# Kernel tuning notes

Hardware: AMD Instinct MI355X
Metric: run time of the kernel (lower is better)

Reference implementation:

```python
import jax, jax.numpy as jnp
import numpy as np

N_ING, N_DIR = 100000, 50000
E = 1000000
H, D = 4, 16          # heads, per-head dim
HID = H * D           # 64
LAT, COND = 32, 8
F_ING, F_DIR = 16, 8
OUT_ING = 16


def _han_edge(x_src, x_dst, att_s, att_d, edge_index, n_dst):
    # HANConv per-edge-type attention message passing.
    src, dst = edge_index[0], edge_index[1]
    a = jax.nn.leaky_relu(
        jnp.einsum('nhd,hd->nh', x_src, att_s)[src]
        + jnp.einsum('nhd,hd->nh', x_dst, att_d)[dst],
        negative_slope=0.2)                               # [E, H]
    amax = jax.ops.segment_max(a, dst, num_segments=n_dst)
    ex = jnp.exp(a - amax[dst])
    denom = jax.ops.segment_sum(ex, dst, num_segments=n_dst)
    alpha = ex / (denom[dst] + 1e-16)                     # PyG softmax eps
    out = jax.ops.segment_sum(x_src[src] * alpha[:, :, None], dst,
                              num_segments=n_dst)         # [n_dst, H, D]
    return jax.nn.relu(out.reshape(n_dst, HID))


def _group(outs, q, Wk, bk):
    # HANConv semantic-level attention across edge types.
    s = jnp.stack(outs)                                   # [T, N, HID]
    score = jnp.tanh(s @ Wk + bk).mean(axis=1) @ q        # [T]
    attn = jax.nn.softmax(score)
    return jnp.einsum('t,tnf->nf', attn, s)


def setup_inputs() -> dict:
    key = jax.random.key(0)
    ks = jax.random.split(key, 32)
    def ei(k, n_src, n_dst):
        k1, k2 = jax.random.split(k)
        return jnp.stack([jax.random.randint(k1, (E,), 0, n_src),
                          jax.random.randint(k2, (E,), 0, n_dst)]).astype(jnp.int64)
    s = 0.1
    inp = {
        'x_ing': jax.random.normal(ks[0], (N_ING, F_ING), jnp.float32),
        'x_dir': jax.random.normal(ks[1], (N_DIR, F_DIR), jnp.float32),
        'cond':  jax.random.normal(ks[2], (COND,), jnp.float32),
        'eps':   jax.random.normal(ks[3], (1, LAT), jnp.float32),
        'ei_cooc':     ei(ks[4], N_ING, N_DIR),
        'ei_used':     ei(ks[5], N_ING, N_DIR),
        'ei_contains': ei(ks[6], N_DIR, N_ING),
        'ei_pairs':    ei(ks[7], N_DIR, N_DIR),
        'ei_follows':  ei(ks[8], N_DIR, N_DIR),
        # node-type projections
        'W_pi': jax.random.normal(ks[9],  (F_ING, HID)) * s,
        'b_pi': jnp.zeros((HID,)),
        'W_pd': jax.random.normal(ks[10], (F_DIR, HID)) * s,
        'b_pd': jnp.zeros((HID,)),
        # semantic attention
        'Wk': jax.random.normal(ks[21], (HID, HID)) * s,
        'bk': jnp.zeros((HID,)),
        'q':  jax.random.normal(ks[22], (HID,)) * s,
        # VAE heads (input: 2*HID + COND)
        'W_mu': jax.random.normal(ks[23], (2 * HID + COND, LAT)) * s,
        'b_mu': jnp.zeros((LAT,)),
        'W_lv': jax.random.normal(ks[24], (2 * HID + COND, LAT)) * s,
        'b_lv': jnp.zeros((LAT,)),
        # decoder (fc1 is dead code in the original forward)
        'W_fc3': jax.random.normal(ks[25], (LAT, HID)) * s,
        'b_fc3': jnp.zeros((HID,)),
        'W_fc2': jax.random.normal(ks[26], (HID, OUT_ING)) * s,
        'b_fc2': jnp.zeros((OUT_ING,)),
    }
    for i, name in enumerate(['cooc', 'used', 'contains', 'pairs', 'follows']):
        inp[f'as_{name}'] = jax.random.normal(ks[11 + i], (H, D)) * s
        inp[f'ad_{name}'] = jax.random.normal(ks[16 + i], (H, D)) * s
    return inp


def reference(x_ing, x_dir, cond, eps,
              ei_cooc, ei_used, ei_contains, ei_pairs, ei_follows,
              W_pi, b_pi, W_pd, b_pd,
              as_cooc, ad_cooc, as_used, ad_used, as_contains, ad_contains,
              as_pairs, ad_pairs, as_follows, ad_follows,
              Wk, bk, q, W_mu, b_mu, W_lv, b_lv,
              W_fc3, b_fc3, W_fc2, b_fc2):
    # node-type projections -> [N, H, D]
    h_ing = (x_ing @ W_pi + b_pi).reshape(N_ING, H, D)
    h_dir = (x_dir @ W_pd + b_pd).reshape(N_DIR, H, D)

    o_cooc = _han_edge(h_ing, h_dir, as_cooc, ad_cooc, ei_cooc, N_DIR)
    o_used = _han_edge(h_ing, h_dir, as_used, ad_used, ei_used, N_DIR)
    o_cont = _han_edge(h_dir, h_ing, as_contains, ad_contains, ei_contains, N_ING)
    o_pair = _han_edge(h_dir, h_dir, as_pairs, ad_pairs, ei_pairs, N_DIR)
    o_foll = _han_edge(h_dir, h_dir, as_follows, ad_follows, ei_follows, N_DIR)

    out_ing = _group([o_cont], q, Wk, bk)                       # [N_ING, HID]
    out_dir = _group([o_cooc, o_used, o_pair, o_foll], q, Wk, bk)

    ingre_pool = out_ing.mean(axis=0, keepdims=True)            # [1, HID]
    direc_pool = out_dir.mean(axis=0, keepdims=True)
    graph_repr = jnp.concatenate([ingre_pool, direc_pool, cond[None]], axis=1)

    mu = graph_repr @ W_mu + b_mu
    logvar = graph_repr @ W_lv + b_lv
    z = mu + eps * jnp.exp(0.5 * logvar)

    # decoder: fc1 branch is overwritten in the original; effective path below
    recon = jnp.tanh(jax.nn.relu(z @ W_fc3 + b_fc3) @ W_fc2 + b_fc2)  # [1, OUT_ING]
    return recon, mu, logvar
```

## Files before the change

### kernel.cpp

```cpp
#include <hip/hip_runtime.h>
#include <hip/hip_fp16.h>
#include <math.h>

#define N_ING 100000
#define N_DIR 50000
#define NE    1000000
#define NDST_TOTAL 300000
#define NBUCK 586
#define BSH   9
#define BMSK  511
#define BA    64
#define NBK   (5 * BA)
#define I4PT  (NE / 4)
#define PB_ING 384
#define PB_DIR 192
#define BPAIR_CAP (5 * NE + 16 * NBUCK)
#define LOG2E 1.442695041f

typedef float v2f __attribute__((ext_vector_type(2)));
typedef __attribute__((ext_vector_type(8))) short bf16x8;
typedef __attribute__((ext_vector_type(4))) float f32x4;

__global__ __launch_bounds__(256) void kA_kernel(
    const int* __restrict__ e0, const int* __restrict__ e1,
    const int* __restrict__ e2, const int* __restrict__ e3,
    const int* __restrict__ e4, int* __restrict__ blockcnt,
    const float* __restrict__ x_ing, const float* __restrict__ W_pi,
    const float* __restrict__ b_pi,
    const float* __restrict__ as_cooc, const float* __restrict__ as_used,
    const float* __restrict__ ad_contains,
    unsigned* __restrict__ h8_ing, __half* __restrict__ s_ing,
    const float* __restrict__ x_dir, const float* __restrict__ W_pd,
    const float* __restrict__ b_pd,
    const float* __restrict__ ad_cooc, const float* __restrict__ ad_used,
    const float* __restrict__ as_contains, const float* __restrict__ as_pairs,
    const float* __restrict__ ad_pairs, const float* __restrict__ as_follows,
    const float* __restrict__ ad_follows,
    unsigned* __restrict__ h8_dir, __half* __restrict__ s_dir)
{
    __shared__ int hist[NBUCK];
    __shared__ float sW[16 * 64];
    __shared__ float sbb[64];
    __shared__ float satt[7 * 64];
    __shared__ float sx[4][16];
    __shared__ float srow[4][64];

    const int bid = blockIdx.x;
    const int tid = threadIdx.x;
    if (bid < NBK) {
        const int type = bid / BA, blk = bid % BA;
        const int* ei = type == 0 ? e0 : type == 1 ? e1 : type == 2 ? e2
                      : type == 3 ? e3 : e4;
        const int base = type == 0 ? 0 : type == 1 ? 50000 : type == 2 ? 100000
                       : type == 3 ? 200000 : 250000;
        for (int i = tid; i < NBUCK; i += 256) hist[i] = 0;
        __syncthreads();
        const int4* d4 = (const int4*)(ei + NE);
        for (int i = blk * 256 + tid; i < I4PT; i += BA * 256) {
            int4 d = d4[i];
            atomicAdd(&hist[(base + d.x) >> BSH], 1);
            atomicAdd(&hist[(base + d.y) >> BSH], 1);
            atomicAdd(&hist[(base + d.z) >> BSH], 1);
            atomicAdd(&hist[(base + d.w) >> BSH], 1);
        }
        __syncthreads();
        int* row = blockcnt + (size_t)bid * NBUCK;
        for (int i = tid; i < NBUCK; i += 256) row[i] = hist[i];
    } else if (bid < NBK + PB_ING) {
        const int g = tid >> 6, t = tid & 63;
        for (int i = tid; i < 16 * 64; i += 256) sW[i] = W_pi[i];
        if (tid < 64) {
            sbb[tid] = b_pi[tid];
            satt[tid]       = as_cooc[tid] * LOG2E;
            satt[64 + tid]  = as_used[tid] * LOG2E;
            satt[128 + tid] = ad_contains[tid] * LOG2E;
        }
        __syncthreads();
        for (int q = bid - NBK; q < N_ING / 4; q += PB_ING) {
            int n = q * 4 + g;
            if (t < 16) sx[g][t] = x_ing[(size_t)n * 16 + t];
            __syncthreads();
            float s = sbb[t];
#pragma unroll
            for (int i = 0; i < 16; ++i) s += sx[g][i] * sW[i * 64 + t];
            srow[g][t] = s;
            __syncthreads();
            if (t < 16) {
                int w0 = __builtin_amdgcn_cvt_pk_fp8_f32(srow[g][t * 4], srow[g][t * 4 + 1], 0, false);
                int w  = __builtin_amdgcn_cvt_pk_fp8_f32(srow[g][t * 4 + 2], srow[g][t * 4 + 3], w0, true);
                h8_ing[(size_t)n * 16 + t] = (unsigned)w;
            }
            if (t < 12) {
                int slot = t >> 2, hh = t & 3;
                float sc = 0.f;
#pragma unroll
                for (int d = 0; d < 16; ++d)
                    sc += srow[g][hh * 16 + d] * satt[slot * 64 + hh * 16 + d];
                s_ing[(size_t)n * 12 + t] = __float2half(sc);
            }
            __syncthreads();
        }
    } else {
        const int g = tid >> 6, t = tid & 63;
        for (int i = tid; i < 8 * 64; i += 256) sW[i] = W_pd[i];
        if (tid < 64) {
            sbb[tid] = b_pd[tid];
            satt[tid]        = ad_cooc[tid] * LOG2E;
            satt[64  + tid]  = ad_used[tid] * LOG2E;
            satt[128 + tid]  = as_contains[tid] * LOG2E;
            satt[192 + tid]  = as_pairs[tid] * LOG2E;
            satt[256 + tid]  = ad_pairs[tid] * LOG2E;
            satt[320 + tid]  = as_follows[tid] * LOG2E;
            satt[384 + tid]  = ad_follows[tid] * LOG2E;
        }
        __syncthreads();
        for (int q = bid - NBK - PB_ING; q < N_DIR / 4; q += PB_DIR) {
            int n = q * 4 + g;
            if (t < 8) sx[g][t] = x_dir[(size_t)n * 8 + t];
            __syncthreads();
            float s = sbb[t];
#pragma unroll
            for (int i = 0; i < 8; ++i) s += sx[g][i] * sW[i * 64 + t];
            srow[g][t] = s;
            __syncthreads();
            if (t < 16) {
                int w0 = __builtin_amdgcn_cvt_pk_fp8_f32(srow[g][t * 4], srow[g][t * 4 + 1], 0, false);
                int w  = __builtin_amdgcn_cvt_pk_fp8_f32(srow[g][t * 4 + 2], srow[g][t * 4 + 3], w0, true);
                h8_dir[(size_t)n * 16 + t] = (unsigned)w;
            }
            if (t < 28) {
                int slot = t >> 2, hh = t & 3;
                float sc = 0.f;
#pragma unroll
                for (int d = 0; d < 16; ++d)
                    sc += srow[g][hh * 16 + d] * satt[slot * 64 + hh * 16 + d];
                s_dir[(size_t)n * 28 + t] = __float2half(sc);
            }
            __syncthreads();
        }
    }
}

__global__ __launch_bounds__(256) void k2_kernel(
    const int* __restrict__ blockcnt, int* __restrict__ blockbase,
    int* __restrict__ bbase, int* __restrict__ btot, int* __restrict__ cursor)
{
    __shared__ int part[4][64];
    __shared__ int tots[64];
    __shared__ int scn[64];
    __shared__ int bw;
    const int tid = threadIdx.x;
    const int kq = tid >> 6, bl = tid & 63;
    const int b = blockIdx.x * 64 + bl;
    const int K = NBK / 4;
    int ps = 0;
    if (b < NBUCK)
        for (int k = kq * K; k < kq * K + K; ++k)
            ps += blockcnt[(size_t)k * NBUCK + b];
    part[kq][bl] = ps;
    __syncthreads();
    if (tid < 64) {
        int t = part[0][tid] + part[1][tid] + part[2][tid] + part[3][tid];
        tots[tid] = t;
        scn[tid] = (t + 15) & ~15;
    }
    __syncthreads();
    for (int off = 1; off < 64; off <<= 1) {
        int v = 0;
        if (tid < 64 && tid >= off) v = scn[tid - off];
        __syncthreads();
        if (tid < 64) scn[tid] += v;
        __syncthreads();
    }
    if (tid == 63) bw = atomicAdd(cursor, scn[63]);
    __syncthreads();
    if (b < NBUCK) {
        int pad = (tots[bl] + 15) & ~15;
        int bs = bw + scn[bl] - pad;
        if (kq == 0) {
            bbase[b] = bs;
            btot[b] = tots[bl];
        }
        int run = bs;
        for (int q = 0; q < kq; ++q) run += part[q][bl];
        for (int k = kq * K; k < kq * K + K; ++k) {
            blockbase[(size_t)k * NBUCK + b] = run;
            run += blockcnt[(size_t)k * NBUCK + b];
        }
    }
}

__global__ __launch_bounds__(256) void k3_kernel(
    const int* __restrict__ e0, const int* __restrict__ e1,
    const int* __restrict__ e2, const int* __restrict__ e3,
    const int* __restrict__ e4, const int* __restrict__ blockbase,
    unsigned* __restrict__ bpair)
{
    __shared__ int cur[NBUCK];
    const int bid = blockIdx.x, tid = threadIdx.x;
    const int type = bid / BA, blk = bid % BA;
    const int* ei = type == 0 ? e0 : type == 1 ? e1 : type == 2 ? e2
                  : type == 3 ? e3 : e4;
    const int base = type == 0 ? 0 : type == 1 ? 50000 : type == 2 ? 100000
                   : type == 3 ? 200000 : 250000;
    const int* row = blockbase + (size_t)bid * NBUCK;
    for (int i = tid; i < NBUCK; i += 256) cur[i] = row[i];
    __syncthreads();
    const int4* s4 = (const int4*)ei;
    const int4* d4 = (const int4*)(ei + NE);
    for (int i = blk * 256 + tid; i < I4PT; i += BA * 256) {
        int4 s = s4[i];
        int4 d = d4[i];
        int g0 = base + d.x, g1 = base + d.y, g2 = base + d.z, g3 = base + d.w;
        int p0 = atomicAdd(&cur[g0 >> BSH], 1);
        int p1 = atomicAdd(&cur[g1 >> BSH], 1);
        int p2 = atomicAdd(&cur[g2 >> BSH], 1);
        int p3 = atomicAdd(&cur[g3 >> BSH], 1);
        bpair[p0] = ((unsigned)(g0 & BMSK) << 17) | (unsigned)s.x;
        bpair[p1] = ((unsigned)(g1 & BMSK) << 17) | (unsigned)s.y;
        bpair[p2] = ((unsigned)(g2 & BMSK) << 17) | (unsigned)s.z;
        bpair[p3] = ((unsigned)(g3 & BMSK) << 17) | (unsigned)s.w;
    }
}

__global__ __launch_bounds__(256) void k4_kernel(
    const unsigned* __restrict__ bpair, const int* __restrict__ bbase,
    const int* __restrict__ btot, int* __restrict__ perm,
    int* __restrict__ start, int* __restrict__ cnt)
{
    __shared__ int h[512], cu[512];
    __shared__ int ts[256];
    const int b = blockIdx.x, tid = threadIdx.x;
    const int jb = bbase[b], n = btot[b];
    h[tid] = 0;
    h[tid + 256] = 0;
    __syncthreads();
    for (int i = tid; i < n; i += 256)
        atomicAdd(&h[bpair[jb + i] >> 17], 1);
    __syncthreads();
    int v0 = h[2 * tid], v1 = h[2 * tid + 1];
    ts[tid] = v0 + v1;
    __syncthreads();
    for (int off = 1; off < 256; off <<= 1) {
        int t2 = 0;
        if (tid >= off) t2 = ts[tid - off];
        __syncthreads();
        ts[tid] += t2;
        __syncthreads();
    }
    int ex = ts[tid] - (v0 + v1);
    cu[2 * tid] = ex;
    cu[2 * tid + 1] = ex + v0;
    int dg = b * 512 + 2 * tid;
    if (dg < NDST_TOTAL) { start[dg] = jb + ex; cnt[dg] = v0; }
    if (dg + 1 < NDST_TOTAL) { start[dg + 1] = jb + ex + v0; cnt[dg + 1] = v1; }
    __syncthreads();
    for (int i = tid; i < n; i += 256) {
        unsigned p = bpair[jb + i];
        int pos = atomicAdd(&cu[p >> 17], 1);
        perm[jb + pos] = (int)(p & 0x1FFFF);
    }
}

__global__ __launch_bounds__(256) void agg_all_kernel(
    const int* __restrict__ perm, const int* __restrict__ start,
    const int* __restrict__ cnttot,
    const unsigned* __restrict__ h8_ing, const unsigned* __restrict__ h8_dir,
    const __half* __restrict__ s_ing, const __half* __restrict__ s_dir,
    unsigned* __restrict__ rows8,
    float* __restrict__ pool_ing, float* __restrict__ pool_dir)
{
    __shared__ __align__(16) float srow[4][64];
    __shared__ float sred[4][64];
    const int t = threadIdx.x & 63, w = threadIdx.x >> 6;
    const int g  = t >> 4;
    const int l4 = t & 15;
    const int hq = l4 >> 2;

    float p_ing = 0.f;
    float p0 = 0.f, p1 = 0.f, p2 = 0.f, p3 = 0.f;
    const int nwaves = gridDim.x * 4;
    for (int d = blockIdx.x * 4 + w; d < NDST_TOTAL; d += nwaves) {
        int type, ld;
        const __half *ssrc, *sdst;
        const unsigned* hsrc;
        unsigned uss, uds; int soff, doff;
        if (d < 50000)       { type = 0; ld = d;          ssrc = s_ing; uss = 12; soff = 0;  sdst = s_dir; uds = 28; doff = 0;  hsrc = h8_ing; }
        else if (d < 100000) { type = 1; ld = d - 50000;  ssrc = s_ing; uss = 12; soff = 4;  sdst = s_dir; uds = 28; doff = 4;  hsrc = h8_ing; }
        else if (d < 200000) { type = 2; ld = d - 100000; ssrc = s_dir; uss = 28; soff = 8;  sdst = s_ing; uds = 12; doff = 8;  hsrc = h8_dir; }
        else if (d < 250000) { type = 3; ld = d - 200000; ssrc = s_dir; uss = 28; soff = 12; sdst = s_dir; uds = 28; doff = 16; hsrc = h8_dir; }
        else                 { type = 4; ld = d - 250000; ssrc = s_dir; uss = 28; soff = 20; sdst = s_dir; uds = 28; doff = 24; hsrc = h8_dir; }
        float adst = __half2float(sdst[(unsigned)ld * uds + (unsigned)(doff + hq)]);
        const unsigned usoff = (unsigned)(soff + hq);
        int jb = start[d], je = jb + cnttot[d];
        int jl = je - 1;
        float4 acc = make_float4(0.f, 0.f, 0.f, 0.f);
        float dsum = 0.f;
        for (int j = jb; j < je; j += 16) {
            int j0 = j + g, j1 = j + 4 + g, j2 = j + 8 + g, j3 = j + 12 + g;
            bool v0 = j0 < je, v1 = j1 < je, v2 = j2 < je, v3 = j3 < je;
            unsigned s0 = (unsigned)perm[v0 ? j0 : jl];
            unsigned s1 = (unsigned)perm[v1 ? j1 : jl];
            unsigned s2 = (unsigned)perm[v2 ? j2 : jl];
            unsigned s3 = (unsigned)perm[v3 ? j3 : jl];
            float c0 = __half2float(ssrc[s0 * uss + usoff]);
            float c1 = __half2float(ssrc[s1 * uss + usoff]);
            float c2 = __half2float(ssrc[s2 * uss + usoff]);
            float c3 = __half2float(ssrc[s3 * uss + usoff]);
            unsigned u0 = hsrc[s0 * 16u + (unsigned)l4];
            unsigned u1 = hsrc[s1 * 16u + (unsigned)l4];
            unsigned u2 = hsrc[s2 * 16u + (unsigned)l4];
            unsigned u3 = hsrc[s3 * 16u + (unsigned)l4];
            float a0 = c0 + adst; a0 = a0 > 0.f ? a0 : 0.2f * a0;
            float a1 = c1 + adst; a1 = a1 > 0.f ? a1 : 0.2f * a1;
            float a2 = c2 + adst; a2 = a2 > 0.f ? a2 : 0.2f * a2;
            float a3 = c3 + adst; a3 = a3 > 0.f ? a3 : 0.2f * a3;
            float e0 = v0 ? __builtin_amdgcn_exp2f(a0) : 0.f;
            float e1 = v1 ? __builtin_amdgcn_exp2f(a1) : 0.f;
            float e2 = v2 ? __builtin_amdgcn_exp2f(a2) : 0.f;
            float e3 = v3 ? __builtin_amdgcn_exp2f(a3) : 0.f;
            dsum += (e0 + e1) + (e2 + e3);
            v2f lo0 = __builtin_amdgcn_cvt_pk_f32_fp8((int)u0, false);
            v2f hi0 = __builtin_amdgcn_cvt_pk_f32_fp8((int)u0, true);
            v2f lo1 = __builtin_amdgcn_cvt_pk_f32_fp8((int)u1, false);
            v2f hi1 = __builtin_amdgcn_cvt_pk_f32_fp8((int)u1, true);
            v2f lo2 = __builtin_amdgcn_cvt_pk_f32_fp8((int)u2, false);
            v2f hi2 = __builtin_amdgcn_cvt_pk_f32_fp8((int)u2, true);
            v2f lo3 = __builtin_amdgcn_cvt_pk_f32_fp8((int)u3, false);
            v2f hi3 = __builtin_amdgcn_cvt_pk_f32_fp8((int)u3, true);
            acc.x += (lo0.x * e0 + lo1.x * e1) + (lo2.x * e2 + lo3.x * e3);
            acc.y += (lo0.y * e0 + lo1.y * e1) + (lo2.y * e2 + lo3.y * e3);
            acc.z += (hi0.x * e0 + hi1.x * e1) + (hi2.x * e2 + hi3.x * e3);
            acc.w += (hi0.y * e0 + hi1.y * e1) + (hi2.y * e2 + hi3.y * e3);
        }
#pragma unroll
        for (int mask = 16; mask <= 32; mask <<= 1) {
            acc.x += __shfl_xor(acc.x, mask, 64);
            acc.y += __shfl_xor(acc.y, mask, 64);
            acc.z += __shfl_xor(acc.z, mask, 64);
            acc.w += __shfl_xor(acc.w, mask, 64);
            dsum  += __shfl_xor(dsum,  mask, 64);
        }
        float inv = 1.f / (dsum + 1e-16f);
        float4 v4 = make_float4(fmaxf(acc.x * inv, 0.f), fmaxf(acc.y * inv, 0.f),
                                fmaxf(acc.z * inv, 0.f), fmaxf(acc.w * inv, 0.f));
        if (g == 0) *(float4*)&srow[w][l4 * 4] = v4;
        float v = srow[w][t];
        if (type == 2) {
            p_ing += v;
        } else {
            if (type == 0)      p0 += v;
            else if (type == 1) p1 += v;
            else if (type == 3) p2 += v;
            else                p3 += v;
            if (g == 0) {
                unsigned md = (unsigned)(d < 100000 ? d : d - 100000);
                int r0 = __builtin_amdgcn_cvt_pk_fp8_f32(v4.x, v4.y, 0, false);
                int r1 = __builtin_amdgcn_cvt_pk_fp8_f32(v4.z, v4.w, r0, true);
                rows8[md * 16u + (unsigned)l4] = (unsigned)r1;
            }
        }
    }
    float vals[5] = { p_ing, p0, p1, p2, p3 };
    float* outs[5] = { pool_ing, pool_dir, pool_dir + 64, pool_dir + 128,
                       pool_dir + 192 };
    for (int i = 0; i < 5; ++i) {
        __syncthreads();
        sred[w][t] = vals[i];
        __syncthreads();
        if (w == 0)
            atomicAdd(&outs[i][t], sred[0][t] + sred[1][t] + sred[2][t] + sred[3][t]);
    }
}

__global__ __launch_bounds__(256) void sem_kernel(
    const unsigned* __restrict__ rows8, const float* __restrict__ Wk,
    const float* __restrict__ bk, float* __restrict__ sem_dir)
{
    __shared__ float swk[4096];
    __shared__ float ssem[256];
    const int tid = threadIdx.x;
    for (int i = tid; i < 4096; i += 256) swk[i] = Wk[i];
    ssem[tid] = 0.f;
    __syncthreads();

    const int lane = tid & 63, w = tid >> 6;
    const int col = lane & 15, kg = lane >> 4;

    bf16x8 bfr[4][2];
    float biasv[4];
#pragma unroll
    for (int nt = 0; nt < 4; ++nt) {
        biasv[nt] = bk[nt * 16 + col];
#pragma unroll
        for (int ks = 0; ks < 2; ++ks) {
            bf16x8 bb;
#pragma unroll
            for (int j = 0; j < 8; ++j) {
                int k = ks * 32 + kg * 8 + j;
                unsigned u = __builtin_bit_cast(unsigned, swk[k * 64 + nt * 16 + col]);
                u = u + 0x7FFFu + ((u >> 16) & 1u);
                bb[j] = (short)(u >> 16);
            }
            bfr[nt][ks] = bb;
        }
    }

    const int gw = blockIdx.x * 4 + w;
    const int nw = gridDim.x * 4;
    for (int tile = gw; tile < 12500; tile += nw) {
        const int tt = tile / 3125;
        const unsigned* rp = rows8 + (unsigned)(tile * 16 + col) * 16u;
        bf16x8 afr[2];
#pragma unroll
        for (int ks = 0; ks < 2; ++ks) {
            uint2 uu = *(const uint2*)(rp + ks * 8 + kg * 2);
            v2f l0 = __builtin_amdgcn_cvt_pk_f32_fp8((int)uu.x, false);
            v2f h0 = __builtin_amdgcn_cvt_pk_f32_fp8((int)uu.x, true);
            v2f l1 = __builtin_amdgcn_cvt_pk_f32_fp8((int)uu.y, false);
            v2f h1 = __builtin_amdgcn_cvt_pk_f32_fp8((int)uu.y, true);
            bf16x8 aa;
            aa[0] = (short)(__builtin_bit_cast(unsigned, l0.x) >> 16);
            aa[1] = (short)(__builtin_bit_cast(unsigned, l0.y) >> 16);
            aa[2] = (short)(__builtin_bit_cast(unsigned, h0.x) >> 16);
            aa[3] = (short)(__builtin_bit_cast(unsigned, h0.y) >> 16);
            aa[4] = (short)(__builtin_bit_cast(unsigned, l1.x) >> 16);
            aa[5] = (short)(__builtin_bit_cast(unsigned, l1.y) >> 16);
            aa[6] = (short)(__builtin_bit_cast(unsigned, h1.x) >> 16);
            aa[7] = (short)(__builtin_bit_cast(unsigned, h1.y) >> 16);
            afr[ks] = aa;
        }
#pragma unroll
        for (int nt = 0; nt < 4; ++nt) {
            f32x4 acc = {0.f, 0.f, 0.f, 0.f};
            acc = __builtin_amdgcn_mfma_f32_16x16x32_bf16(afr[0], bfr[nt][0], acc, 0, 0, 0);
            acc = __builtin_amdgcn_mfma_f32_16x16x32_bf16(afr[1], bfr[nt][1], acc, 0, 0, 0);
            float s = 0.f;
#pragma unroll
            for (int reg = 0; reg < 4; ++reg) {
                float x = acc[reg] + biasv[nt];
                x = fminf(fmaxf(x, -15.f), 15.f);
                float e = __builtin_amdgcn_exp2f(x * (2.f * LOG2E));
                s += (e - 1.f) * __builtin_amdgcn_rcpf(e + 1.f);
            }
            s += __shfl_xor(s, 16, 64);
            s += __shfl_xor(s, 32, 64);
            if (lane < 16) atomicAdd(&ssem[tt * 64 + nt * 16 + col], s);
        }
    }
    __syncthreads();
    atomicAdd(&sem_dir[tid], ssem[tid]);
}

__global__ __launch_bounds__(64) void final_kernel(
    const float* __restrict__ pool_ing, const float* __restrict__ pool_dir,
    const float* __restrict__ sem_dir, const float* __restrict__ q,
    const float* __restrict__ cond, const float* __restrict__ eps,
    const float* __restrict__ W_mu, const float* __restrict__ b_mu,
    const float* __restrict__ W_lv, const float* __restrict__ b_lv,
    const float* __restrict__ W_fc3, const float* __restrict__ b_fc3,
    const float* __restrict__ W_fc2, const float* __restrict__ b_fc2,
    float* __restrict__ out)
{
    __shared__ float gr[136];
    __shared__ float sc[4], attn[4];
    __shared__ float z[32], hfc[64];
    int t = threadIdx.x;
    if (t < 4) {
        float s = 0.f;
        for (int f = 0; f < 64; ++f)
            s += (sem_dir[t * 64 + f] / (float)N_DIR) * q[f];
        sc[t] = s;
    }
    gr[t] = pool_ing[t] / (float)N_ING;
    __syncthreads();
    if (t == 0) {
        float m = fmaxf(fmaxf(sc[0], sc[1]), fmaxf(sc[2], sc[3]));
        float ssum = 0.f;
        for (int i = 0; i < 4; ++i) { attn[i] = expf(sc[i] - m); ssum += attn[i]; }
        for (int i = 0; i < 4; ++i) attn[i] /= ssum;
    }
    __syncthreads();
    {
        float v = 0.f;
        for (int tt = 0; tt < 4; ++tt)
            v += attn[tt] * (pool_dir[tt * 64 + t] / (float)N_DIR);
        gr[64 + t] = v;
    }
    if (t < 8) gr[128 + t] = cond[t];
    __syncthreads();
    if (t < 32) {
        float m = b_mu[t], lv = b_lv[t];
        for (int i = 0; i < 136; ++i) {
            float g = gr[i];
            m  += g * W_mu[i * 32 + t];
            lv += g * W_lv[i * 32 + t];
        }
        out[16 + t] = m;
        out[48 + t] = lv;
        z[t] = m + eps[t] * expf(0.5f * lv);
    }
    __syncthreads();
    {
        float v = b_fc3[t];
        for (int j = 0; j < 32; ++j) v += z[j] * W_fc3[j * 64 + t];
        hfc[t] = fmaxf(v, 0.f);
    }
    __syncthreads();
    if (t < 16) {
        float v = b_fc2[t];
        for (int f = 0; f < 64; ++f) v += hfc[f] * W_fc2[f * 16 + t];
        out[t] = tanhf(v);
    }
}

extern "C" void kernel_launch(void* const* d_in, const int* in_sizes, int n_in,
                              void* d_out, int out_size, void* d_ws, size_t ws_size,
                              hipStream_t stream) {
    const float* x_ing = (const float*)d_in[0];
    const float* x_dir = (const float*)d_in[1];
    const float* cond  = (const float*)d_in[2];
    const float* eps   = (const float*)d_in[3];
    const int* ei_cooc     = (const int*)d_in[4];
    const int* ei_used     = (const int*)d_in[5];
    const int* ei_contains = (const int*)d_in[6];
    const int* ei_pairs    = (const int*)d_in[7];
    const int* ei_follows  = (const int*)d_in[8];
    const float* W_pi = (const float*)d_in[9];
    const float* b_pi = (const float*)d_in[10];
    const float* W_pd = (const float*)d_in[11];
    const float* b_pd = (const float*)d_in[12];
    const float* Wk   = (const float*)d_in[13];
    const float* bk   = (const float*)d_in[14];
    const float* q    = (const float*)d_in[15];
    const float* W_mu = (const float*)d_in[16];
    const float* b_mu = (const float*)d_in[17];
    const float* W_lv = (const float*)d_in[18];
    const float* b_lv = (const float*)d_in[19];
    const float* W_fc3 = (const float*)d_in[20];
    const float* b_fc3 = (const float*)d_in[21];
    const float* W_fc2 = (const float*)d_in[22];
    const float* b_fc2 = (const float*)d_in[23];
    const float* as_cooc     = (const float*)d_in[24];
    const float* ad_cooc     = (const float*)d_in[25];
    const float* as_used     = (const float*)d_in[26];
    const float* ad_used     = (const float*)d_in[27];
    const float* as_contains = (const float*)d_in[28];
    const float* ad_contains = (const float*)d_in[29];
    const float* as_pairs    = (const float*)d_in[30];
    const float* ad_pairs    = (const float*)d_in[31];
    const float* as_follows  = (const float*)d_in[32];
    const float* ad_follows  = (const float*)d_in[33];

    unsigned* bpair = (unsigned*)d_ws;
    unsigned* h8_ing = bpair + (size_t)BPAIR_CAP;
    unsigned* h8_dir = h8_ing + (size_t)N_ING * 16;
    __half* s_ing = (__half*)(h8_dir + (size_t)N_DIR * 16);
    __half* s_dir = s_ing + (size_t)N_ING * 12;
    int*   perm  = (int*)(s_dir + (size_t)N_DIR * 28);
    int*   bbase  = perm + (size_t)BPAIR_CAP;
    int*   btot   = bbase + NBUCK;
    int*   start  = btot + NBUCK;
    int*   cnt    = start + NDST_TOTAL;
    int*   cursor = cnt + NDST_TOTAL;
    float* pool_ing = (float*)(cursor + 1);
    float* pool_dir = pool_ing + 64;
    float* sem_dir  = pool_dir + 256;
    unsigned* rows8 = bpair;
    int* blockcnt  = (int*)bpair;
    int* blockbase = (int*)perm;

    hipMemsetAsync(cursor, 0, (1 + 64 + 256 + 256) * sizeof(int), stream);

    kA_kernel<<<NBK + PB_ING + PB_DIR, 256, 0, stream>>>(
        ei_cooc, ei_used, ei_contains, ei_pairs, ei_follows, blockcnt,
        x_ing, W_pi, b_pi, as_cooc, as_used, ad_contains, h8_ing, s_ing,
        x_dir, W_pd, b_pd, ad_cooc, ad_used, as_contains, as_pairs, ad_pairs,
        as_follows, ad_follows, h8_dir, s_dir);

    k2_kernel<<<(NBUCK + 63) / 64, 256, 0, stream>>>(
        blockcnt, blockbase, bbase, btot, cursor);

    k3_kernel<<<NBK, 256, 0, stream>>>(
        ei_cooc, ei_used, ei_contains, ei_pairs, ei_follows, blockbase, bpair);

    k4_kernel<<<NBUCK, 256, 0, stream>>>(bpair, bbase, btot, perm, start, cnt);

    agg_all_kernel<<<2048, 256, 0, stream>>>(
        perm, start, cnt, h8_ing, h8_dir, s_ing, s_dir, rows8,
        pool_ing, pool_dir);

    sem_kernel<<<512, 256, 0, stream>>>(rows8, Wk, bk, sem_dir);

    final_kernel<<<1, 64, 0, stream>>>(
        pool_ing, pool_dir, sem_dir, q, cond, eps,
        W_mu, b_mu, W_lv, b_lv, W_fc3, b_fc3, W_fc2, b_fc2, (float*)d_out);
}
```

Measured before the change: 491.6 us.

## Split histogram into 1024-thread kernel and widen scatter and bucket-sort blocks

Moves the edge-destination histogram out of the fused projection kernel into its own kernel with 1024-thread blocks, and raises k3's scatter blocks to 1024 threads and k4's per-bucket sort blocks to 512 threads (one thread per destination slot). The aim is more latency hiding and fewer loop iterations per block in the memory- and atomic-bound sorting stages. The cost is an extra kernel launch, the loss of overlap between histogram and projection work, and more LDS atomic contention per block plus more barriers in the larger k4 scan.

```diff
diff --git a/kernel.cpp b/kernel.cpp
--- a/kernel.cpp
+++ b/kernel.cpp
@@ -21,10 +21,35 @@
 typedef __attribute__((ext_vector_type(8))) short bf16x8;
 typedef __attribute__((ext_vector_type(4))) float f32x4;
 
-__global__ __launch_bounds__(256) void kA_kernel(
+__global__ __launch_bounds__(1024) void k0_hist(
     const int* __restrict__ e0, const int* __restrict__ e1,
     const int* __restrict__ e2, const int* __restrict__ e3,
-    const int* __restrict__ e4, int* __restrict__ blockcnt,
+    const int* __restrict__ e4, int* __restrict__ blockcnt)
+{
+    __shared__ int hist[NBUCK];
+    const int bid = blockIdx.x;
+    const int tid = threadIdx.x;
+    const int type = bid / BA, blk = bid % BA;
+    const int* ei = type == 0 ? e0 : type == 1 ? e1 : type == 2 ? e2
+                  : type == 3 ? e3 : e4;
+    const int base = type == 0 ? 0 : type == 1 ? 50000 : type == 2 ? 100000
+                   : type == 3 ? 200000 : 250000;
+    for (int i = tid; i < NBUCK; i += 1024) hist[i] = 0;
+    __syncthreads();
+    const int4* d4 = (const int4*)(ei + NE);
+    for (int i = blk * 1024 + tid; i < I4PT; i += BA * 1024) {
+        int4 d = d4[i];
+        atomicAdd(&hist[(base + d.x) >> BSH], 1);
+        atomicAdd(&hist[(base + d.y) >> BSH], 1);
+        atomicAdd(&hist[(base + d.z) >> BSH], 1);
+        atomicAdd(&hist[(base + d.w) >> BSH], 1);
+    }
+    __syncthreads();
+    int* row = blockcnt + (size_t)bid * NBUCK;
+    for (int i = tid; i < NBUCK; i += 1024) row[i] = hist[i];
+}
+
+__global__ __launch_bounds__(256) void kA_kernel(
     const float* __restrict__ x_ing, const float* __restrict__ W_pi,
     const float* __restrict__ b_pi,
     const float* __restrict__ as_cooc, const float* __restrict__ as_used,
@@ -38,7 +63,6 @@
     const float* __restrict__ ad_follows,
     unsigned* __restrict__ h8_dir, __half* __restrict__ s_dir)
 {
-    __shared__ int hist[NBUCK];
     __shared__ float sW[16 * 64];
     __shared__ float sbb[64];
     __shared__ float satt[7 * 64];
@@ -47,26 +71,7 @@
 
     const int bid = blockIdx.x;
     const int tid = threadIdx.x;
-    if (bid < NBK) {
-        const int type = bid / BA, blk = bid % BA;
-        const int* ei = type == 0 ? e0 : type == 1 ? e1 : type == 2 ? e2
-                      : type == 3 ? e3 : e4;
-        const int base = type == 0 ? 0 : type == 1 ? 50000 : type == 2 ? 100000
-                       : type == 3 ? 200000 : 250000;
-        for (int i = tid; i < NBUCK; i += 256) hist[i] = 0;
-        __syncthreads();
-        const int4* d4 = (const int4*)(ei + NE);
-        for (int i = blk * 256 + tid; i < I4PT; i += BA * 256) {
-            int4 d = d4[i];
-            atomicAdd(&hist[(base + d.x) >> BSH], 1);
-            atomicAdd(&hist[(base + d.y) >> BSH], 1);
-            atomicAdd(&hist[(base + d.z) >> BSH], 1);
-            atomicAdd(&hist[(base + d.w) >> BSH], 1);
-        }
-        __syncthreads();
-        int* row = blockcnt + (size_t)bid * NBUCK;
-        for (int i = tid; i < NBUCK; i += 256) row[i] = hist[i];
-    } else if (bid < NBK + PB_ING) {
+    if (bid < PB_ING) {
         const int g = tid >> 6, t = tid & 63;
         for (int i = tid; i < 16 * 64; i += 256) sW[i] = W_pi[i];
         if (tid < 64) {
@@ -76,7 +81,7 @@
             satt[128 + tid] = ad_contains[tid] * LOG2E;
         }
         __syncthreads();
-        for (int q = bid - NBK; q < N_ING / 4; q += PB_ING) {
+        for (int q = bid; q < N_ING / 4; q += PB_ING) {
             int n = q * 4 + g;
             if (t < 16) sx[g][t] = x_ing[(size_t)n * 16 + t];
             __syncthreads();
@@ -114,7 +119,7 @@
             satt[384 + tid]  = ad_follows[tid] * LOG2E;
         }
         __syncthreads();
-        for (int q = bid - NBK - PB_ING; q < N_DIR / 4; q += PB_DIR) {
+        for (int q = bid - PB_ING; q < N_DIR / 4; q += PB_DIR) {
             int n = q * 4 + g;
             if (t < 8) sx[g][t] = x_dir[(size_t)n * 8 + t];
             __syncthreads();
@@ -190,7 +195,7 @@
     }
 }
 
-__global__ __launch_bounds__(256) void k3_kernel(
+__global__ __launch_bounds__(1024) void k3_kernel(
     const int* __restrict__ e0, const int* __restrict__ e1,
     const int* __restrict__ e2, const int* __restrict__ e3,
     const int* __restrict__ e4, const int* __restrict__ blockbase,
@@ -204,11 +209,11 @@
     const int base = type == 0 ? 0 : type == 1 ? 50000 : type == 2 ? 100000
                    : type == 3 ? 200000 : 250000;
     const int* row = blockbase + (size_t)bid * NBUCK;
-    for (int i = tid; i < NBUCK; i += 256) cur[i] = row[i];
+    for (int i = tid; i < NBUCK; i += 1024) cur[i] = row[i];
     __syncthreads();
     const int4* s4 = (const int4*)ei;
     const int4* d4 = (const int4*)(ei + NE);
-    for (int i = blk * 256 + tid; i < I4PT; i += BA * 256) {
+    for (int i = blk * 1024 + tid; i < I4PT; i += BA * 1024) {
         int4 s = s4[i];
         int4 d = d4[i];
         int g0 = base + d.x, g1 = base + d.y, g2 = base + d.z, g3 = base + d.w;
@@ -223,39 +228,35 @@
     }
 }
 
-__global__ __launch_bounds__(256) void k4_kernel(
+__global__ __launch_bounds__(512) void k4_kernel(
     const unsigned* __restrict__ bpair, const int* __restrict__ bbase,
     const int* __restrict__ btot, int* __restrict__ perm,
     int* __restrict__ start, int* __restrict__ cnt)
 {
-    __shared__ int h[512], cu[512];
-    __shared__ int ts[256];
+    __shared__ int h[512], cu[512], sc[512];
     const int b = blockIdx.x, tid = threadIdx.x;
     const int jb = bbase[b], n = btot[b];
     h[tid] = 0;
-    h[tid + 256] = 0;
-    __syncthreads();
-    for (int i = tid; i < n; i += 256)
+    __syncthreads();
+    for (int i = tid; i < n; i += 512)
         atomicAdd(&h[bpair[jb + i] >> 17], 1);
     __syncthreads();
-    int v0 = h[2 * tid], v1 = h[2 * tid + 1];
-    ts[tid] = v0 + v1;
-    __syncthreads();
-    for (int off = 1; off < 256; off <<= 1) {
+    int v = h[tid];
+    sc[tid] = v;
+    __syncthreads();
+    for (int off = 1; off < 512; off <<= 1) {
         int t2 = 0;
-        if (tid >= off) t2 = ts[tid - off];
-        __syncthreads();
-        ts[tid] += t2;
-        __syncthreads();
-    }
-    int ex = ts[tid] - (v0 + v1);
-    cu[2 * tid] = ex;
-    cu[2 * tid + 1] = ex + v0;
-    int dg = b * 512 + 2 * tid;
-    if (dg < NDST_TOTAL) { start[dg] = jb + ex; cnt[dg] = v0; }
-    if (dg + 1 < NDST_TOTAL) { start[dg + 1] = jb + ex + v0; cnt[dg + 1] = v1; }
-    __syncthreads();
-    for (int i = tid; i < n; i += 256) {
+        if (tid >= off) t2 = sc[tid - off];
+        __syncthreads();
+        sc[tid] += t2;
+        __syncthreads();
+    }
+    int ex = sc[tid] - v;
+    cu[tid] = ex;
+    int dg = b * 512 + tid;
+    if (dg < NDST_TOTAL) { start[dg] = jb + ex; cnt[dg] = v; }
+    __syncthreads();
+    for (int i = tid; i < n; i += 512) {
         unsigned p = bpair[jb + i];
         int pos = atomicAdd(&cu[p >> 17], 1);
         perm[jb + pos] = (int)(p & 0x1FFFF);
@@ -572,8 +573,10 @@
 
     hipMemsetAsync(cursor, 0, (1 + 64 + 256 + 256) * sizeof(int), stream);
 
-    kA_kernel<<<NBK + PB_ING + PB_DIR, 256, 0, stream>>>(
-        ei_cooc, ei_used, ei_contains, ei_pairs, ei_follows, blockcnt,
+    k0_hist<<<NBK, 1024, 0, stream>>>(
+        ei_cooc, ei_used, ei_contains, ei_pairs, ei_follows, blockcnt);
+
+    kA_kernel<<<PB_ING + PB_DIR, 256, 0, stream>>>(
         x_ing, W_pi, b_pi, as_cooc, as_used, ad_contains, h8_ing, s_ing,
         x_dir, W_pd, b_pd, ad_cooc, ad_used, as_contains, as_pairs, ad_pairs,
         as_follows, ad_follows, h8_dir, s_dir);
@@ -581,10 +584,10 @@
     k2_kernel<<<(NBUCK + 63) / 64, 256, 0, stream>>>(
         blockcnt, blockbase, bbase, btot, cursor);
 
-    k3_kernel<<<NBK, 256, 0, stream>>>(
+    k3_kernel<<<NBK, 1024, 0, stream>>>(
         ei_cooc, ei_used, ei_contains, ei_pairs, ei_follows, blockbase, bpair);
 
-    k4_kernel<<<NBUCK, 256, 0, stream>>>(bpair, bbase, btot, perm, start, cnt);
+    k4_kernel<<<NBUCK, 512, 0, stream>>>(bpair, bbase, btot, perm, start, cnt);
 
     agg_all_kernel<<<2048, 256, 0, stream>>>(
         perm, start, cnt, h8_ing, h8_dir, s_ing, s_dir, rows8,
```

Measured after the change: 493.7 us. Within noise of the previous version (+0.4%).
